# Optimization experiments

Hardware: AMD Instinct MI355X
Metric: run time of the kernel (lower is better)

The kernel has to match this reference:

```python
import jax, jax.numpy as jnp
import numpy as np

E, B, D, H, Z = 8, 16384, 512, 512, 64   # experts, batch, input_dim, hidden, latent
NHID = 2                                 # num_mlp_layers - 1 hidden-to-hidden layers


def setup_inputs() -> dict:
    key = jax.random.key(0)
    ks = jax.random.split(key, 12)

    def w(k, shape, fan_in):
        return (jax.random.normal(k, shape, jnp.float32) / np.sqrt(fan_in)).astype(jnp.float32)

    return {
        "x": jax.random.normal(ks[0], (B, D), jnp.float32),
        "eps": jax.random.normal(ks[1], (B, Z), jnp.float32),
        # stacked per-expert parameters (leading axis E)
        "enc_in_w": w(ks[2], (E, D, H), D), "enc_in_b": jnp.zeros((E, H), jnp.float32),
        "enc_hid_w": w(ks[3], (E, NHID, H, H), H), "enc_hid_b": jnp.zeros((E, NHID, H), jnp.float32),
        "mu_w": w(ks[4], (E, H, Z), H), "mu_b": jnp.zeros((E, Z), jnp.float32),
        "lv_w": w(ks[5], (E, H, Z), H), "lv_b": jnp.zeros((E, Z), jnp.float32),
        "dec_in_w": w(ks[6], (E, Z, H), Z), "dec_in_b": jnp.zeros((E, H), jnp.float32),
        "dec_hid_w": w(ks[7], (E, NHID, H, H), H), "dec_hid_b": jnp.zeros((E, NHID, H), jnp.float32),
        "dec_out_w": w(ks[8], (E, H, D), H), "dec_out_b": jnp.zeros((E, D), jnp.float32),
    }


def _moe_forward(x, eps, enc_in_w, enc_in_b, enc_hid_w, enc_hid_b,
                 mu_w, mu_b, lv_w, lv_b,
                 dec_in_w, dec_in_b, dec_hid_w, dec_hid_b, dec_out_w, dec_out_b):
    # ---- every expert tries the problem (dense, all experts over full batch) ----
    h = jax.nn.relu(jnp.einsum('bd,edh->ebh', x, enc_in_w) + enc_in_b[:, None, :])
    for i in range(NHID):
        h = jax.nn.relu(jnp.einsum('ebh,ehk->ebk', h, enc_hid_w[:, i]) + enc_hid_b[:, i, None, :])
    mu = jnp.einsum('ebh,ehz->ebz', h, mu_w) + mu_b[:, None, :]          # [E,B,Z]
    logvar = jnp.einsum('ebh,ehz->ebz', h, lv_w) + lv_b[:, None, :]       # [E,B,Z]
    z = mu + jnp.exp(0.5 * logvar) * eps[None, :, :]                      # reparameterize
    g = jax.nn.relu(jnp.einsum('ebz,ezh->ebh', z, dec_in_w) + dec_in_b[:, None, :])
    for i in range(NHID):
        g = jax.nn.relu(jnp.einsum('ebh,ehk->ebk', g, dec_hid_w[:, i]) + dec_hid_b[:, i, None, :])
    xhat = jnp.einsum('ebh,ehd->ebd', g, dec_out_w) + dec_out_b[:, None, :]  # [E,B,D]

    # ---- per-sample recon loss, pick best expert (torch.min over experts) ----
    recon = jnp.mean((xhat - x[None, :, :]) ** 2, axis=-1)                # [E,B]
    expert_idx = jnp.argmin(recon, axis=0)                                # [B]

    # ---- sparse_others: single fused gather instead of python loop ----
    bi = jnp.arange(x.shape[0])
    return mu[expert_idx, bi], logvar[expert_idx, bi], xhat[expert_idx, bi]


def reference(x, eps, enc_in_w, enc_in_b, enc_hid_w, enc_hid_b,
              mu_w, mu_b, lv_w, lv_b,
              dec_in_w, dec_in_b, dec_hid_w, dec_hid_b, dec_out_w, dec_out_b):
    return _moe_forward(x, eps, enc_in_w, enc_in_b, enc_hid_w, enc_hid_b,
                        mu_w, mu_b, lv_w, lv_b,
                        dec_in_w, dec_in_b, dec_hid_w, dec_hid_b, dec_out_w, dec_out_b)
```

## Files before the change

### kernel.cpp

```cpp
#include <hip/hip_runtime.h>
#include <cstdint>

#define Eexp 8
#define Bb   16384
#define Dd   512
#define Hh   512
#define Zz   64

typedef _Float16 f16x8 __attribute__((ext_vector_type(8)));
typedef float    f32x4 __attribute__((ext_vector_type(4)));

#define OFF_ENCIN  0
#define OFF_HID0   524288
#define OFF_HID1   1048576
#define OFF_HEADS  1572864
#define OFF_DECIN  1703936
#define OFF_DHID0  1769472
#define OFF_DHID1  2293760
#define OFF_DECOUT 2818048
#define PEREXP     3342336
#define WT_TOTAL   (8 * (size_t)PEREXP)

#define GLL16(g, l) __builtin_amdgcn_global_load_lds( \
    (const __attribute__((address_space(1))) void*)(g), \
    (__attribute__((address_space(3))) void*)(l), 16, 0, 0)

template<bool TR>
__global__ __launch_bounds__(256)
void fmsplit(const float* __restrict__ src, _Float16* __restrict__ dst,
             int KTOT, int inner, long sStride, long dStride)
{
    __shared__ float t[64][65];
    const int e  = blockIdx.z;
    const int o0 = blockIdx.x * 64;
    const int k0 = blockIdx.y * 64;
    const float* S = src + (size_t)e * sStride;
    _Float16*    D = dst + (size_t)e * dStride;
    const int tid = threadIdx.x;
    const int rr = tid >> 4, c4 = (tid & 15) * 4;
    #pragma unroll
    for (int p = 0; p < 4; ++p) {
        const int r = rr + p * 16;
        const float4 v = *reinterpret_cast<const float4*>(
            S + (size_t)(TR ? (k0 + r) : (o0 + r)) * inner + (TR ? o0 : k0) + c4);
        t[r][c4 + 0] = v.x; t[r][c4 + 1] = v.y;
        t[r][c4 + 2] = v.z; t[r][c4 + 3] = v.w;
    }
    __syncthreads();
    const int lane = tid & 63, wid = tid >> 6;
    const int KB = KTOT >> 5;
    #pragma unroll
    for (int p = 0; p < 2; ++p) {
        const int g  = wid * 2 + p;
        const int ot = g >> 1, kb = g & 1;
        const int rI = ot * 16 + (lane & 15);
        const int kI = kb * 32 + (lane >> 4) * 8;
        f16x8 hv, lv;
        #pragma unroll
        for (int j = 0; j < 8; ++j) {
            const float v = TR ? t[kI + j][rI] : t[rI][kI + j];
            const _Float16 h = (_Float16)v;
            hv[j] = h; lv[j] = (_Float16)(v - (float)h);
        }
        const size_t base = ((size_t)((o0 >> 4) + ot) * KB + (k0 >> 5) + kb) * 1024;
        *reinterpret_cast<f16x8*>(D + base + lane * 8)       = hv;
        *reinterpret_cast<f16x8*>(D + base + 512 + lane * 8) = lv;
    }
}

__global__ __launch_bounds__(256)
void zfm_kernel(const float* __restrict__ mu, const float* __restrict__ lv,
                const float* __restrict__ eps, _Float16* __restrict__ zfm)
{
    __shared__ float t[64][65];
    const int r0 = blockIdx.x * 64;
    const int tid = threadIdx.x, rr = tid >> 4, c4 = (tid & 15) * 4;
    #pragma unroll
    for (int p = 0; p < 4; ++p) {
        const int r = rr + p * 16;
        const size_t o = (size_t)(r0 + r) * 64 + c4;
        const float4 m = *reinterpret_cast<const float4*>(mu + o);
        const float4 l = *reinterpret_cast<const float4*>(lv + o);
        const float4 e = *reinterpret_cast<const float4*>(eps + o);
        t[r][c4 + 0] = m.x + expf(0.5f * l.x) * e.x;
        t[r][c4 + 1] = m.y + expf(0.5f * l.y) * e.y;
        t[r][c4 + 2] = m.z + expf(0.5f * l.z) * e.z;
        t[r][c4 + 3] = m.w + expf(0.5f * l.w) * e.w;
    }
    __syncthreads();
    const int lane = tid & 63, wid = tid >> 6;
    #pragma unroll
    for (int p = 0; p < 2; ++p) {
        const int g  = wid * 2 + p;
        const int ot = g >> 1, kb = g & 1;
        const int rI = ot * 16 + (lane & 15);
        const int kI = kb * 32 + (lane >> 4) * 8;
        f16x8 hv, lvv;
        #pragma unroll
        for (int j = 0; j < 8; ++j) {
            const float v = t[rI][kI + j];
            const _Float16 h = (_Float16)v;
            hv[j] = h; lvv[j] = (_Float16)(v - (float)h);
        }
        const size_t base = ((size_t)((r0 >> 4) + ot) * 2 + kb) * 1024;
        *reinterpret_cast<f16x8*>(zfm + base + lane * 8)       = hv;
        *reinterpret_cast<f16x8*>(zfm + base + 512 + lane * 8) = lvv;
    }
}

template<int KA, int MODE>
__global__ __launch_bounds__(256, 2)
void gemm11(const _Float16* __restrict__ Afm, const _Float16* __restrict__ Wfm,
            const float* __restrict__ bias0, const float* __restrict__ bias1,
            float* __restrict__ Cf, float* __restrict__ Cf1,
            _Float16* __restrict__ Cfm, const float* __restrict__ Xin,
            float* __restrict__ rec8)
{
    constexpr bool BIG = (MODE != 2);
    constexpr int MF  = BIG ? 4 : 2;
    constexpr int KB  = KA / 32;
    constexpr int NT  = KB;
    constexpr int ACH = BIG ? 16 : 8;
    constexpr int NCH = ACH + 16;
    constexpr int GPW = NCH / 4;
    __shared__ __align__(16) _Float16 lds[2 * NCH * 512];

    const int bid = blockIdx.x;
    int bx, by;
    if (BIG) { bx = (bid & 7) * 16 + (bid >> 5); by = (bid >> 3) & 3; }
    else     { bx = (bid & 7) * 32 + (bid >> 3); by = 0; }

    const int lane = threadIdx.x & 63, wid = threadIdx.x >> 6;
    const int wr = wid >> 1, wc = wid & 1;
    const int row0 = bx * (BIG ? 128 : 64);
    const int col0 = by * 128;

    const _Float16* src[GPW];
    #pragma unroll
    for (int p = 0; p < GPW; ++p) {
        const int q = wid * GPW + p;
        if (q < ACH)
            src[p] = Afm + (size_t)((row0 >> 4) + (q >> 1)) * KB * 1024
                         + (q & 1) * 512 + lane * 8;
        else {
            const int qq = q - ACH;
            src[p] = Wfm + (size_t)((col0 >> 4) + (qq >> 1)) * KB * 1024
                         + (qq & 1) * 512 + lane * 8;
        }
    }

    f32x4 acc[MF][4];
    #pragma unroll
    for (int i = 0; i < MF; ++i)
        #pragma unroll
        for (int j = 0; j < 4; ++j) acc[i][j] = {0.f, 0.f, 0.f, 0.f};

#define STAGE(buf)                                                           \
    { _Pragma("unroll")                                                      \
      for (int p = 0; p < GPW; ++p) {                                        \
          GLL16(src[p], lds + (buf) * (NCH * 512) + (wid * GPW + p) * 512);  \
          src[p] += 1024;                                                    \
      } }

    STAGE(0)
    if (NT > 1) STAGE(1)

    for (int t = 0; t < NT; ++t) {
        if (t + 1 < NT) { asm volatile("s_waitcnt vmcnt(%0)" :: "i"(GPW) : "memory"); }
        else            { asm volatile("s_waitcnt vmcnt(0)" ::: "memory"); }
        __builtin_amdgcn_s_barrier();
        asm volatile("" ::: "memory");

        const _Float16* B0 = lds + (t & 1) * (NCH * 512);
        f16x8 ah[MF], al[MF], wh[4], wl[4];
        #pragma unroll
        for (int mf = 0; mf < MF; ++mf) {
            const int q = (wr * MF + mf) * 2;
            ah[mf] = *reinterpret_cast<const f16x8*>(B0 + q * 512 + lane * 8);
            al[mf] = *reinterpret_cast<const f16x8*>(B0 + q * 512 + 512 + lane * 8);
        }
        #pragma unroll
        for (int nf = 0; nf < 4; ++nf) {
            const int q = ACH + (wc * 4 + nf) * 2;
            wh[nf] = *reinterpret_cast<const f16x8*>(B0 + q * 512 + lane * 8);
            wl[nf] = *reinterpret_cast<const f16x8*>(B0 + q * 512 + 512 + lane * 8);
        }
        __builtin_amdgcn_s_setprio(1);
        #pragma unroll
        for (int mf = 0; mf < MF; ++mf)
            #pragma unroll
            for (int nf = 0; nf < 4; ++nf) {
                acc[mf][nf] = __builtin_amdgcn_mfma_f32_16x16x32_f16(
                    ah[mf], wh[nf], acc[mf][nf], 0, 0, 0);
                acc[mf][nf] = __builtin_amdgcn_mfma_f32_16x16x32_f16(
                    ah[mf], wl[nf], acc[mf][nf], 0, 0, 0);
                acc[mf][nf] = __builtin_amdgcn_mfma_f32_16x16x32_f16(
                    al[mf], wh[nf], acc[mf][nf], 0, 0, 0);
            }
        __builtin_amdgcn_s_setprio(0);
        asm volatile("" ::: "memory");
        __builtin_amdgcn_s_barrier();
        asm volatile("" ::: "memory");
        if (t + 2 < NT) STAGE(t & 1)
    }
#undef STAGE

    if constexpr (MODE == 0) {
        uint32_t* sb = reinterpret_cast<uint32_t*>(&lds[0]);
        #pragma unroll
        for (int ph = 0; ph < 2; ++ph) {
            if (wc == ph) {
                #pragma unroll
                for (int nf = 0; nf < 4; ++nf) {
                    const int c_l = nf * 16 + (lane & 15);
                    const float bv = bias0[col0 + ph * 64 + c_l];
                    #pragma unroll
                    for (int mf = 0; mf < 4; ++mf)
                        #pragma unroll
                        for (int j = 0; j < 4; ++j) {
                            const int r_l = wr * 64 + mf * 16 + (lane >> 4) * 4 + j;
                            const float v = fmaxf(acc[mf][nf][j] + bv, 0.f);
                            const _Float16 h = (_Float16)v;
                            const _Float16 lo = (_Float16)(v - (float)h);
                            const uint32_t pk =
                                (uint32_t)__builtin_bit_cast(uint16_t, h) |
                                ((uint32_t)__builtin_bit_cast(uint16_t, lo) << 16);
                            sb[r_l * 64 + (((c_l >> 2) ^ (r_l & 15)) << 2) + (c_l & 3)] = pk;
                        }
                }
            }
            __syncthreads();
            {
                #pragma unroll
                for (int i = 0; i < 4; ++i) {
                    const int q = wid * 4 + i;
                    const int T_l = q >> 1, kb_l = q & 1;
                    const int r_l = T_l * 16 + (lane & 15);
                    const int cb  = kb_l * 32 + (lane >> 4) * 8;
                    uint32_t u[8];
                    #pragma unroll
                    for (int jb = 0; jb < 2; ++jb) {
                        const int chunk = ((cb >> 2) + jb) ^ (r_l & 15);
                        const uint32_t* pp = &sb[r_l * 64 + chunk * 4];
                        u[jb*4+0] = pp[0]; u[jb*4+1] = pp[1];
                        u[jb*4+2] = pp[2]; u[jb*4+3] = pp[3];
                    }
                    f16x8 hv, lvv;
                    #pragma unroll
                    for (int j = 0; j < 8; ++j) {
                        hv[j]  = __builtin_bit_cast(_Float16, (uint16_t)(u[j] & 0xffff));
                        lvv[j] = __builtin_bit_cast(_Float16, (uint16_t)(u[j] >> 16));
                    }
                    const size_t base =
                        ((size_t)((row0 >> 4) + T_l) * 16 +
                         ((col0 + ph * 64) >> 5) + kb_l) * 1024;
                    *reinterpret_cast<f16x8*>(Cfm + base + lane * 8)       = hv;
                    *reinterpret_cast<f16x8*>(Cfm + base + 512 + lane * 8) = lvv;
                }
            }
            __syncthreads();
        }
    } else if constexpr (MODE == 1) {
        float rsum[4][4];
        #pragma unroll
        for (int mf = 0; mf < 4; ++mf)
            #pragma unroll
            for (int j = 0; j < 4; ++j) rsum[mf][j] = 0.f;
        #pragma unroll
        for (int nf = 0; nf < 4; ++nf) {
            const int col = col0 + wc * 64 + nf * 16 + (lane & 15);
            const float bv = bias0[col];
            #pragma unroll
            for (int mf = 0; mf < 4; ++mf)
                #pragma unroll
                for (int j = 0; j < 4; ++j) {
                    const int row = row0 + wr * 64 + mf * 16 + (lane >> 4) * 4 + j;
                    const float v = acc[mf][nf][j] + bv;
                    Cf[(size_t)row * 512 + col] = v;
                    const float d = v - Xin[(size_t)row * 512 + col];
                    rsum[mf][j] += d * d;
                }
        }
        #pragma unroll
        for (int mf = 0; mf < 4; ++mf)
            #pragma unroll
            for (int j = 0; j < 4; ++j) {
                float s = rsum[mf][j];
                s += __shfl_xor(s, 1); s += __shfl_xor(s, 2);
                s += __shfl_xor(s, 4); s += __shfl_xor(s, 8);
                if ((lane & 15) == 0) {
                    const int row = row0 + wr * 64 + mf * 16 + (lane >> 4) * 4 + j;
                    rec8[(size_t)(by * 2 + wc) * Bb + row] = s;
                }
            }
    } else {
        #pragma unroll
        for (int nf = 0; nf < 4; ++nf) {
            const int c_h = wc * 64 + nf * 16 + (lane & 15);
            const float bv = (c_h < 64) ? bias0[c_h] : bias1[c_h - 64];
            float* CP = (c_h < 64) ? Cf : Cf1;
            const int c = c_h & 63;
            #pragma unroll
            for (int mf = 0; mf < MF; ++mf)
                #pragma unroll
                for (int j = 0; j < 4; ++j) {
                    const int row = row0 + wr * 32 + mf * 16 + (lane >> 4) * 4 + j;
                    CP[(size_t)row * 64 + c] = acc[mf][nf][j] + bv;
                }
        }
    }
}

__global__ __launch_bounds__(256)
void select_kernel(const float* __restrict__ rec8, float* __restrict__ best,
                   const float* __restrict__ mu_e, const float* __restrict__ lv_e,
                   const float* __restrict__ xhat,
                   float* __restrict__ out_mu, float* __restrict__ out_lv,
                   float* __restrict__ out_xh, int isFirst)
{
    const int wave = threadIdx.x >> 6;
    const int lane = threadIdx.x & 63;
    const int row  = blockIdx.x * 4 + wave;
    float r = 0.f;
    #pragma unroll
    for (int p = 0; p < 8; ++p) r += rec8[(size_t)p * Bb + row];
    r *= (1.0f / 512.0f);
    const bool cond = isFirst || (r < best[row]);
    if (cond) {
        if (lane == 0) best[row] = r;
        out_mu[(size_t)row * Zz + lane] = mu_e[(size_t)row * Zz + lane];
        out_lv[(size_t)row * Zz + lane] = lv_e[(size_t)row * Zz + lane];
        const float4* src = reinterpret_cast<const float4*>(&xhat[(size_t)row * Dd]);
        float4*       dst = reinterpret_cast<float4*>(&out_xh[(size_t)row * Dd]);
        dst[lane]      = src[lane];
        dst[lane + 64] = src[lane + 64];
    }
}

extern "C" void kernel_launch(void* const* d_in, const int* in_sizes, int n_in,
                              void* d_out, int out_size, void* d_ws, size_t ws_size,
                              hipStream_t stream)
{
    const float* x         = (const float*)d_in[0];
    const float* eps       = (const float*)d_in[1];
    const float* enc_in_w  = (const float*)d_in[2];
    const float* enc_in_b  = (const float*)d_in[3];
    const float* enc_hid_w = (const float*)d_in[4];
    const float* enc_hid_b = (const float*)d_in[5];
    const float* mu_w      = (const float*)d_in[6];
    const float* mu_b      = (const float*)d_in[7];
    const float* lv_w      = (const float*)d_in[8];
    const float* lv_b      = (const float*)d_in[9];
    const float* dec_in_w  = (const float*)d_in[10];
    const float* dec_in_b  = (const float*)d_in[11];
    const float* dec_hid_w = (const float*)d_in[12];
    const float* dec_hid_b = (const float*)d_in[13];
    const float* dec_out_w = (const float*)d_in[14];
    const float* dec_out_b = (const float*)d_in[15];

    const size_t FM = (size_t)Bb * 512 * 2;
    const size_t BZ = (size_t)Bb * 64;

    _Float16* wt  = (_Float16*)d_ws;
    _Float16* xfm = wt + WT_TOTAL;
    _Float16* afm = xfm + FM;
    _Float16* bfm = afm + FM;
    _Float16* zfm = bfm + FM;
    float* fbase  = (float*)(zfm + (size_t)Bb * 64 * 2);
    float* xhat   = fbase;
    float* mu_e   = xhat + (size_t)Bb * 512;
    float* lv_e   = mu_e + BZ;
    float* rec8   = lv_e + BZ;
    float* best   = rec8 + (size_t)8 * Bb;

    float* out_mu = (float*)d_out;
    float* out_lv = out_mu + (size_t)Bb * Zz;
    float* out_xh = out_lv + (size_t)Bb * Zz;

    const dim3 blk(256);

    fmsplit<true ><<<dim3(8, 8, 8), blk, 0, stream>>>(enc_in_w,           wt + OFF_ENCIN,  512, 512, 262144, PEREXP);
    fmsplit<true ><<<dim3(8, 8, 8), blk, 0, stream>>>(enc_hid_w,          wt + OFF_HID0,   512, 512, 524288, PEREXP);
    fmsplit<true ><<<dim3(8, 8, 8), blk, 0, stream>>>(enc_hid_w + 262144, wt + OFF_HID1,   512, 512, 524288, PEREXP);
    fmsplit<true ><<<dim3(1, 8, 8), blk, 0, stream>>>(mu_w,               wt + OFF_HEADS,  512,  64,  32768, PEREXP);
    fmsplit<true ><<<dim3(1, 8, 8), blk, 0, stream>>>(lv_w,        wt + OFF_HEADS + 65536, 512,  64,  32768, PEREXP);
    fmsplit<true ><<<dim3(8, 1, 8), blk, 0, stream>>>(dec_in_w,           wt + OFF_DECIN,   64, 512,  32768, PEREXP);
    fmsplit<true ><<<dim3(8, 8, 8), blk, 0, stream>>>(dec_hid_w,          wt + OFF_DHID0,  512, 512, 524288, PEREXP);
    fmsplit<true ><<<dim3(8, 8, 8), blk, 0, stream>>>(dec_hid_w + 262144, wt + OFF_DHID1,  512, 512, 524288, PEREXP);
    fmsplit<true ><<<dim3(8, 8, 8), blk, 0, stream>>>(dec_out_w,          wt + OFF_DECOUT, 512, 512, 262144, PEREXP);
    fmsplit<false><<<dim3(256, 8, 1), blk, 0, stream>>>(x,                xfm,             512, 512, 0, 0);

    const dim3 g512(512), g256(256), gRow(Bb / 4), gZ(Bb / 64);

    for (int e = 0; e < Eexp; ++e) {
        const _Float16* we = wt + (size_t)e * PEREXP;
        gemm11<512, 0><<<g512, blk, 0, stream>>>(
            xfm, we + OFF_ENCIN, enc_in_b + (size_t)e * Hh, nullptr,
            nullptr, nullptr, afm, nullptr, nullptr);
        gemm11<512, 0><<<g512, blk, 0, stream>>>(
            afm, we + OFF_HID0, enc_hid_b + ((size_t)e * 2 + 0) * Hh, nullptr,
            nullptr, nullptr, bfm, nullptr, nullptr);
        gemm11<512, 0><<<g512, blk, 0, stream>>>(
            bfm, we + OFF_HID1, enc_hid_b + ((size_t)e * 2 + 1) * Hh, nullptr,
            nullptr, nullptr, afm, nullptr, nullptr);
        gemm11<512, 2><<<g256, blk, 0, stream>>>(
            afm, we + OFF_HEADS, mu_b + (size_t)e * Zz, lv_b + (size_t)e * Zz,
            mu_e, lv_e, nullptr, nullptr, nullptr);
        zfm_kernel<<<gZ, blk, 0, stream>>>(mu_e, lv_e, eps, zfm);
        gemm11< 64, 0><<<g512, blk, 0, stream>>>(
            zfm, we + OFF_DECIN, dec_in_b + (size_t)e * Hh, nullptr,
            nullptr, nullptr, bfm, nullptr, nullptr);
        gemm11<512, 0><<<g512, blk, 0, stream>>>(
            bfm, we + OFF_DHID0, dec_hid_b + ((size_t)e * 2 + 0) * Hh, nullptr,
            nullptr, nullptr, afm, nullptr, nullptr);
        gemm11<512, 0><<<g512, blk, 0, stream>>>(
            afm, we + OFF_DHID1, dec_hid_b + ((size_t)e * 2 + 1) * Hh, nullptr,
            nullptr, nullptr, bfm, nullptr, nullptr);
        gemm11<512, 1><<<g512, blk, 0, stream>>>(
            bfm, we + OFF_DECOUT, dec_out_b + (size_t)e * Dd, nullptr,
            xhat, nullptr, nullptr, x, rec8);
        select_kernel<<<gRow, blk, 0, stream>>>(
            rec8, best, mu_e, lv_e, xhat, out_mu, out_lv, out_xh, e == 0 ? 1 : 0);
    }
}
```

Baseline: 1.737 ms.

## Fuse reparameterization into heads GEMM and argmin-select into decoder output GEMM

Folds the z = mu + exp(0.5*logvar)*eps step and its fp16 hi/lo split into the heads GEMM epilogue, which removes the separate zfm kernel and a re-read of mu/logvar. The decoder output GEMM now uses 512-thread blocks that each cover a full 64x512 row slab. This lets it compute per-row reconstruction error in-block, compare against the running best, and write the winning xhat, mu and logvar directly. The fp32 xhat and rec8 intermediates and the select kernel are dropped, cutting global traffic and launches per expert. The cost is a new tile shape and a serial per-row copy loop for mu/lv in two waves.

```diff
diff --git a/kernel.cpp b/kernel.cpp
--- a/kernel.cpp
+++ b/kernel.cpp
@@ -68,71 +68,25 @@
     }
 }
 
-__global__ __launch_bounds__(256)
-void zfm_kernel(const float* __restrict__ mu, const float* __restrict__ lv,
-                const float* __restrict__ eps, _Float16* __restrict__ zfm)
+template<int KA>
+__global__ __launch_bounds__(256, 2)
+void gemm_mid(const _Float16* __restrict__ Afm, const _Float16* __restrict__ Wfm,
+              const float* __restrict__ bias0, _Float16* __restrict__ Cfm)
 {
-    __shared__ float t[64][65];
-    const int r0 = blockIdx.x * 64;
-    const int tid = threadIdx.x, rr = tid >> 4, c4 = (tid & 15) * 4;
-    #pragma unroll
-    for (int p = 0; p < 4; ++p) {
-        const int r = rr + p * 16;
-        const size_t o = (size_t)(r0 + r) * 64 + c4;
-        const float4 m = *reinterpret_cast<const float4*>(mu + o);
-        const float4 l = *reinterpret_cast<const float4*>(lv + o);
-        const float4 e = *reinterpret_cast<const float4*>(eps + o);
-        t[r][c4 + 0] = m.x + expf(0.5f * l.x) * e.x;
-        t[r][c4 + 1] = m.y + expf(0.5f * l.y) * e.y;
-        t[r][c4 + 2] = m.z + expf(0.5f * l.z) * e.z;
-        t[r][c4 + 3] = m.w + expf(0.5f * l.w) * e.w;
-    }
-    __syncthreads();
-    const int lane = tid & 63, wid = tid >> 6;
-    #pragma unroll
-    for (int p = 0; p < 2; ++p) {
-        const int g  = wid * 2 + p;
-        const int ot = g >> 1, kb = g & 1;
-        const int rI = ot * 16 + (lane & 15);
-        const int kI = kb * 32 + (lane >> 4) * 8;
-        f16x8 hv, lvv;
-        #pragma unroll
-        for (int j = 0; j < 8; ++j) {
-            const float v = t[rI][kI + j];
-            const _Float16 h = (_Float16)v;
-            hv[j] = h; lvv[j] = (_Float16)(v - (float)h);
-        }
-        const size_t base = ((size_t)((r0 >> 4) + ot) * 2 + kb) * 1024;
-        *reinterpret_cast<f16x8*>(zfm + base + lane * 8)       = hv;
-        *reinterpret_cast<f16x8*>(zfm + base + 512 + lane * 8) = lvv;
-    }
-}
-
-template<int KA, int MODE>
-__global__ __launch_bounds__(256, 2)
-void gemm11(const _Float16* __restrict__ Afm, const _Float16* __restrict__ Wfm,
-            const float* __restrict__ bias0, const float* __restrict__ bias1,
-            float* __restrict__ Cf, float* __restrict__ Cf1,
-            _Float16* __restrict__ Cfm, const float* __restrict__ Xin,
-            float* __restrict__ rec8)
-{
-    constexpr bool BIG = (MODE != 2);
-    constexpr int MF  = BIG ? 4 : 2;
     constexpr int KB  = KA / 32;
     constexpr int NT  = KB;
-    constexpr int ACH = BIG ? 16 : 8;
-    constexpr int NCH = ACH + 16;
-    constexpr int GPW = NCH / 4;
+    constexpr int ACH = 16;
+    constexpr int NCH = 32;
+    constexpr int GPW = 8;
     __shared__ __align__(16) _Float16 lds[2 * NCH * 512];
 
     const int bid = blockIdx.x;
-    int bx, by;
-    if (BIG) { bx = (bid & 7) * 16 + (bid >> 5); by = (bid >> 3) & 3; }
-    else     { bx = (bid & 7) * 32 + (bid >> 3); by = 0; }
+    const int bx = (bid & 7) * 16 + (bid >> 5);
+    const int by = (bid >> 3) & 3;
 
     const int lane = threadIdx.x & 63, wid = threadIdx.x >> 6;
     const int wr = wid >> 1, wc = wid & 1;
-    const int row0 = bx * (BIG ? 128 : 64);
+    const int row0 = bx * 128;
     const int col0 = by * 128;
 
     const _Float16* src[GPW];
@@ -149,9 +103,9 @@
         }
     }
 
-    f32x4 acc[MF][4];
-    #pragma unroll
-    for (int i = 0; i < MF; ++i)
+    f32x4 acc[4][4];
+    #pragma unroll
+    for (int i = 0; i < 4; ++i)
         #pragma unroll
         for (int j = 0; j < 4; ++j) acc[i][j] = {0.f, 0.f, 0.f, 0.f};
 
@@ -172,10 +126,10 @@
         asm volatile("" ::: "memory");
 
         const _Float16* B0 = lds + (t & 1) * (NCH * 512);
-        f16x8 ah[MF], al[MF], wh[4], wl[4];
-        #pragma unroll
-        for (int mf = 0; mf < MF; ++mf) {
-            const int q = (wr * MF + mf) * 2;
+        f16x8 ah[4], al[4], wh[4], wl[4];
+        #pragma unroll
+        for (int mf = 0; mf < 4; ++mf) {
+            const int q = (wr * 4 + mf) * 2;
             ah[mf] = *reinterpret_cast<const f16x8*>(B0 + q * 512 + lane * 8);
             al[mf] = *reinterpret_cast<const f16x8*>(B0 + q * 512 + 512 + lane * 8);
         }
@@ -187,7 +141,7 @@
         }
         __builtin_amdgcn_s_setprio(1);
         #pragma unroll
-        for (int mf = 0; mf < MF; ++mf)
+        for (int mf = 0; mf < 4; ++mf)
             #pragma unroll
             for (int nf = 0; nf < 4; ++nf) {
                 acc[mf][nf] = __builtin_amdgcn_mfma_f32_16x16x32_f16(
@@ -205,135 +159,338 @@
     }
 #undef STAGE
 
-    if constexpr (MODE == 0) {
-        uint32_t* sb = reinterpret_cast<uint32_t*>(&lds[0]);
-        #pragma unroll
-        for (int ph = 0; ph < 2; ++ph) {
-            if (wc == ph) {
+    uint32_t* sb = reinterpret_cast<uint32_t*>(&lds[0]);
+    #pragma unroll
+    for (int ph = 0; ph < 2; ++ph) {
+        if (wc == ph) {
+            #pragma unroll
+            for (int nf = 0; nf < 4; ++nf) {
+                const int c_l = nf * 16 + (lane & 15);
+                const float bv = bias0[col0 + ph * 64 + c_l];
                 #pragma unroll
-                for (int nf = 0; nf < 4; ++nf) {
-                    const int c_l = nf * 16 + (lane & 15);
-                    const float bv = bias0[col0 + ph * 64 + c_l];
+                for (int mf = 0; mf < 4; ++mf)
                     #pragma unroll
-                    for (int mf = 0; mf < 4; ++mf)
-                        #pragma unroll
-                        for (int j = 0; j < 4; ++j) {
-                            const int r_l = wr * 64 + mf * 16 + (lane >> 4) * 4 + j;
-                            const float v = fmaxf(acc[mf][nf][j] + bv, 0.f);
-                            const _Float16 h = (_Float16)v;
-                            const _Float16 lo = (_Float16)(v - (float)h);
-                            const uint32_t pk =
-                                (uint32_t)__builtin_bit_cast(uint16_t, h) |
-                                ((uint32_t)__builtin_bit_cast(uint16_t, lo) << 16);
-                            sb[r_l * 64 + (((c_l >> 2) ^ (r_l & 15)) << 2) + (c_l & 3)] = pk;
-                        }
+                    for (int j = 0; j < 4; ++j) {
+                        const int r_l = wr * 64 + mf * 16 + (lane >> 4) * 4 + j;
+                        const float v = fmaxf(acc[mf][nf][j] + bv, 0.f);
+                        const _Float16 h = (_Float16)v;
+                        const _Float16 lo = (_Float16)(v - (float)h);
+                        const uint32_t pk =
+                            (uint32_t)__builtin_bit_cast(uint16_t, h) |
+                            ((uint32_t)__builtin_bit_cast(uint16_t, lo) << 16);
+                        sb[r_l * 64 + (((c_l >> 2) ^ (r_l & 15)) << 2) + (c_l & 3)] = pk;
+                    }
+            }
+        }
+        __syncthreads();
+        {
+            #pragma unroll
+            for (int i = 0; i < 4; ++i) {
+                const int q = wid * 4 + i;
+                const int T_l = q >> 1, kb_l = q & 1;
+                const int r_l = T_l * 16 + (lane & 15);
+                const int cb  = kb_l * 32 + (lane >> 4) * 8;
+                uint32_t u[8];
+                #pragma unroll
+                for (int jb = 0; jb < 2; ++jb) {
+                    const int chunk = ((cb >> 2) + jb) ^ (r_l & 15);
+                    const uint32_t* pp = &sb[r_l * 64 + chunk * 4];
+                    u[jb*4+0] = pp[0]; u[jb*4+1] = pp[1];
+                    u[jb*4+2] = pp[2]; u[jb*4+3] = pp[3];
                 }
-            }
-            __syncthreads();
-            {
+                f16x8 hv, lvv;
                 #pragma unroll
-                for (int i = 0; i < 4; ++i) {
-                    const int q = wid * 4 + i;
-                    const int T_l = q >> 1, kb_l = q & 1;
-                    const int r_l = T_l * 16 + (lane & 15);
-                    const int cb  = kb_l * 32 + (lane >> 4) * 8;
-                    uint32_t u[8];
-                    #pragma unroll
-                    for (int jb = 0; jb < 2; ++jb) {
-                        const int chunk = ((cb >> 2) + jb) ^ (r_l & 15);
-                        const uint32_t* pp = &sb[r_l * 64 + chunk * 4];
-                        u[jb*4+0] = pp[0]; u[jb*4+1] = pp[1];
-                        u[jb*4+2] = pp[2]; u[jb*4+3] = pp[3];
-                    }
-                    f16x8 hv, lvv;
-                    #pragma unroll
-                    for (int j = 0; j < 8; ++j) {
-                        hv[j]  = __builtin_bit_cast(_Float16, (uint16_t)(u[j] & 0xffff));
-                        lvv[j] = __builtin_bit_cast(_Float16, (uint16_t)(u[j] >> 16));
-                    }
-                    const size_t base =
-                        ((size_t)((row0 >> 4) + T_l) * 16 +
-                         ((col0 + ph * 64) >> 5) + kb_l) * 1024;
-                    *reinterpret_cast<f16x8*>(Cfm + base + lane * 8)       = hv;
-                    *reinterpret_cast<f16x8*>(Cfm + base + 512 + lane * 8) = lvv;
+                for (int j = 0; j < 8; ++j) {
+                    hv[j]  = __builtin_bit_cast(_Float16, (uint16_t)(u[j] & 0xffff));
+                    lvv[j] = __builtin_bit_cast(_Float16, (uint16_t)(u[j] >> 16));
                 }
-            }
-            __syncthreads();
-        }
-    } else if constexpr (MODE == 1) {
-        float rsum[4][4];
-        #pragma unroll
-        for (int mf = 0; mf < 4; ++mf)
-            #pragma unroll
-            for (int j = 0; j < 4; ++j) rsum[mf][j] = 0.f;
+                const size_t base =
+                    ((size_t)((row0 >> 4) + T_l) * 16 +
+                     ((col0 + ph * 64) >> 5) + kb_l) * 1024;
+                *reinterpret_cast<f16x8*>(Cfm + base + lane * 8)       = hv;
+                *reinterpret_cast<f16x8*>(Cfm + base + 512 + lane * 8) = lvv;
+            }
+        }
+        __syncthreads();
+    }
+}
+
+__global__ __launch_bounds__(256, 2)
+void heads_z(const _Float16* __restrict__ Afm, const _Float16* __restrict__ Wfm,
+             const float* __restrict__ mu_b, const float* __restrict__ lv_b,
+             const float* __restrict__ eps,
+             float* __restrict__ mu_e, float* __restrict__ lv_e,
+             _Float16* __restrict__ zfm)
+{
+    constexpr int KB = 16, NT = 16, ACH = 8, NCH = 24, GPW = 6;
+    __shared__ __align__(16) _Float16 lds[2 * NCH * 512];
+
+    const int bid = blockIdx.x;
+    const int bx = (bid & 7) * 32 + (bid >> 3);
+    const int lane = threadIdx.x & 63, wid = threadIdx.x >> 6;
+    const int wr = wid >> 1, wc = wid & 1;
+    const int row0 = bx * 64;
+
+    const _Float16* src[GPW];
+    #pragma unroll
+    for (int p = 0; p < GPW; ++p) {
+        const int q = wid * GPW + p;
+        if (q < ACH)
+            src[p] = Afm + (size_t)((row0 >> 4) + (q >> 1)) * KB * 1024
+                         + (q & 1) * 512 + lane * 8;
+        else {
+            const int qq = q - ACH;
+            src[p] = Wfm + (size_t)(qq >> 1) * KB * 1024 + (qq & 1) * 512 + lane * 8;
+        }
+    }
+
+    f32x4 acc[2][4];
+    #pragma unroll
+    for (int i = 0; i < 2; ++i)
+        #pragma unroll
+        for (int j = 0; j < 4; ++j) acc[i][j] = {0.f, 0.f, 0.f, 0.f};
+
+#define STAGE(buf)                                                           \
+    { _Pragma("unroll")                                                      \
+      for (int p = 0; p < GPW; ++p) {                                        \
+          GLL16(src[p], lds + (buf) * (NCH * 512) + (wid * GPW + p) * 512);  \
+          src[p] += 1024;                                                    \
+      } }
+
+    STAGE(0)
+    STAGE(1)
+
+    for (int t = 0; t < NT; ++t) {
+        if (t + 1 < NT) { asm volatile("s_waitcnt vmcnt(%0)" :: "i"(GPW) : "memory"); }
+        else            { asm volatile("s_waitcnt vmcnt(0)" ::: "memory"); }
+        __builtin_amdgcn_s_barrier();
+        asm volatile("" ::: "memory");
+
+        const _Float16* B0 = lds + (t & 1) * (NCH * 512);
+        f16x8 ah[2], al[2], wh[4], wl[4];
+        #pragma unroll
+        for (int mf = 0; mf < 2; ++mf) {
+            const int q = (wr * 2 + mf) * 2;
+            ah[mf] = *reinterpret_cast<const f16x8*>(B0 + q * 512 + lane * 8);
+            al[mf] = *reinterpret_cast<const f16x8*>(B0 + q * 512 + 512 + lane * 8);
+        }
         #pragma unroll
         for (int nf = 0; nf < 4; ++nf) {
-            const int col = col0 + wc * 64 + nf * 16 + (lane & 15);
-            const float bv = bias0[col];
-            #pragma unroll
-            for (int mf = 0; mf < 4; ++mf)
-                #pragma unroll
-                for (int j = 0; j < 4; ++j) {
-                    const int row = row0 + wr * 64 + mf * 16 + (lane >> 4) * 4 + j;
-                    const float v = acc[mf][nf][j] + bv;
-                    Cf[(size_t)row * 512 + col] = v;
-                    const float d = v - Xin[(size_t)row * 512 + col];
-                    rsum[mf][j] += d * d;
-                }
-        }
-        #pragma unroll
-        for (int mf = 0; mf < 4; ++mf)
+            const int q = ACH + (wc * 4 + nf) * 2;
+            wh[nf] = *reinterpret_cast<const f16x8*>(B0 + q * 512 + lane * 8);
+            wl[nf] = *reinterpret_cast<const f16x8*>(B0 + q * 512 + 512 + lane * 8);
+        }
+        __builtin_amdgcn_s_setprio(1);
+        #pragma unroll
+        for (int mf = 0; mf < 2; ++mf)
+            #pragma unroll
+            for (int nf = 0; nf < 4; ++nf) {
+                acc[mf][nf] = __builtin_amdgcn_mfma_f32_16x16x32_f16(
+                    ah[mf], wh[nf], acc[mf][nf], 0, 0, 0);
+                acc[mf][nf] = __builtin_amdgcn_mfma_f32_16x16x32_f16(
+                    ah[mf], wl[nf], acc[mf][nf], 0, 0, 0);
+                acc[mf][nf] = __builtin_amdgcn_mfma_f32_16x16x32_f16(
+                    al[mf], wh[nf], acc[mf][nf], 0, 0, 0);
+            }
+        __builtin_amdgcn_s_setprio(0);
+        asm volatile("" ::: "memory");
+        __builtin_amdgcn_s_barrier();
+        asm volatile("" ::: "memory");
+        if (t + 2 < NT) STAGE(t & 1)
+    }
+#undef STAGE
+
+    float* mulv = reinterpret_cast<float*>(&lds[0]);
+    #pragma unroll
+    for (int nf = 0; nf < 4; ++nf) {
+        const int c_h = wc * 64 + nf * 16 + (lane & 15);
+        const float bv = (c_h < 64) ? mu_b[c_h] : lv_b[c_h - 64];
+        #pragma unroll
+        for (int mf = 0; mf < 2; ++mf)
             #pragma unroll
             for (int j = 0; j < 4; ++j) {
-                float s = rsum[mf][j];
-                s += __shfl_xor(s, 1); s += __shfl_xor(s, 2);
-                s += __shfl_xor(s, 4); s += __shfl_xor(s, 8);
-                if ((lane & 15) == 0) {
-                    const int row = row0 + wr * 64 + mf * 16 + (lane >> 4) * 4 + j;
-                    rec8[(size_t)(by * 2 + wc) * Bb + row] = s;
-                }
-            }
-    } else {
-        #pragma unroll
-        for (int nf = 0; nf < 4; ++nf) {
-            const int c_h = wc * 64 + nf * 16 + (lane & 15);
-            const float bv = (c_h < 64) ? bias0[c_h] : bias1[c_h - 64];
-            float* CP = (c_h < 64) ? Cf : Cf1;
-            const int c = c_h & 63;
-            #pragma unroll
-            for (int mf = 0; mf < MF; ++mf)
-                #pragma unroll
-                for (int j = 0; j < 4; ++j) {
-                    const int row = row0 + wr * 32 + mf * 16 + (lane >> 4) * 4 + j;
-                    CP[(size_t)row * 64 + c] = acc[mf][nf][j] + bv;
-                }
-        }
+                const int r_l = wr * 32 + mf * 16 + (lane >> 4) * 4 + j;
+                mulv[r_l * 128 + c_h] = acc[mf][nf][j] + bv;
+            }
+    }
+    __syncthreads();
+    const int tid = threadIdx.x;
+    #pragma unroll
+    for (int k = 0; k < 16; ++k) {
+        const int id  = tid + k * 256;
+        const int r_l = id >> 6, c = id & 63;
+        const float m = mulv[r_l * 128 + c];
+        const float l = mulv[r_l * 128 + 64 + c];
+        const size_t go = (size_t)(row0 + r_l) * 64 + c;
+        const float ev = eps[go];
+        const float z  = m + expf(0.5f * l) * ev;
+        mu_e[go] = m; lv_e[go] = l;
+        const _Float16 h  = (_Float16)z;
+        const _Float16 lo = (_Float16)(z - (float)h);
+        const size_t base = ((size_t)((row0 + r_l) >> 4) * 2 + (c >> 5)) * 1024
+                            + ((r_l & 15) + ((c >> 3) & 3) * 16) * 8 + (c & 7);
+        zfm[base]       = h;
+        zfm[base + 512] = lo;
     }
 }
 
-__global__ __launch_bounds__(256)
-void select_kernel(const float* __restrict__ rec8, float* __restrict__ best,
+__global__ __launch_bounds__(512, 2)
+void dec_out_fused(const _Float16* __restrict__ Afm, const _Float16* __restrict__ Wfm,
+                   const float* __restrict__ bias,
+                   const float* __restrict__ Xin,
                    const float* __restrict__ mu_e, const float* __restrict__ lv_e,
-                   const float* __restrict__ xhat,
+                   float* __restrict__ best,
                    float* __restrict__ out_mu, float* __restrict__ out_lv,
                    float* __restrict__ out_xh, int isFirst)
 {
-    const int wave = threadIdx.x >> 6;
-    const int lane = threadIdx.x & 63;
-    const int row  = blockIdx.x * 4 + wave;
-    float r = 0.f;
-    #pragma unroll
-    for (int p = 0; p < 8; ++p) r += rec8[(size_t)p * Bb + row];
-    r *= (1.0f / 512.0f);
-    const bool cond = isFirst || (r < best[row]);
-    if (cond) {
-        if (lane == 0) best[row] = r;
-        out_mu[(size_t)row * Zz + lane] = mu_e[(size_t)row * Zz + lane];
-        out_lv[(size_t)row * Zz + lane] = lv_e[(size_t)row * Zz + lane];
-        const float4* src = reinterpret_cast<const float4*>(&xhat[(size_t)row * Dd]);
-        float4*       dst = reinterpret_cast<float4*>(&out_xh[(size_t)row * Dd]);
-        dst[lane]      = src[lane];
-        dst[lane + 64] = src[lane + 64];
+    constexpr int KB = 16, NT = 16, ACH = 8, NCH = 72, GPW = 9;
+    __shared__ __align__(16) _Float16 lds[2 * NCH * 512];
+
+    const int bid = blockIdx.x;
+    const int bx = (bid & 7) * 32 + (bid >> 3);
+    const int lane = threadIdx.x & 63, wid = threadIdx.x >> 6;
+    const int row0 = bx * 64;
+    const int colW = wid * 64;
+
+    const _Float16* src[GPW];
+    #pragma unroll
+    for (int p = 0; p < GPW; ++p) {
+        const int q = wid * GPW + p;
+        if (q < ACH)
+            src[p] = Afm + (size_t)((row0 >> 4) + (q >> 1)) * KB * 1024
+                         + (q & 1) * 512 + lane * 8;
+        else {
+            const int qq = q - ACH;
+            src[p] = Wfm + (size_t)(qq >> 1) * KB * 1024 + (qq & 1) * 512 + lane * 8;
+        }
+    }
+
+    f32x4 acc[4][4];
+    #pragma unroll
+    for (int i = 0; i < 4; ++i)
+        #pragma unroll
+        for (int j = 0; j < 4; ++j) acc[i][j] = {0.f, 0.f, 0.f, 0.f};
+
+#define STAGE(buf)                                                           \
+    { _Pragma("unroll")                                                      \
+      for (int p = 0; p < GPW; ++p) {                                        \
+          GLL16(src[p], lds + (buf) * (NCH * 512) + (wid * GPW + p) * 512);  \
+          src[p] += 1024;                                                    \
+      } }
+
+    STAGE(0)
+    STAGE(1)
+
+    for (int t = 0; t < NT; ++t) {
+        if (t + 1 < NT) { asm volatile("s_waitcnt vmcnt(%0)" :: "i"(GPW) : "memory"); }
+        else            { asm volatile("s_waitcnt vmcnt(0)" ::: "memory"); }
+        __builtin_amdgcn_s_barrier();
+        asm volatile("" ::: "memory");
+
+        const _Float16* B0 = lds + (t & 1) * (NCH * 512);
+        f16x8 ah[4], al[4], wh[4], wl[4];
+        #pragma unroll
+        for (int mf = 0; mf < 4; ++mf) {
+            const int q = mf * 2;
+            ah[mf] = *reinterpret_cast<const f16x8*>(B0 + q * 512 + lane * 8);
+            al[mf] = *reinterpret_cast<const f16x8*>(B0 + q * 512 + 512 + lane * 8);
+        }
+        #pragma unroll
+        for (int nf = 0; nf < 4; ++nf) {
+            const int q = ACH + (wid * 4 + nf) * 2;
+            wh[nf] = *reinterpret_cast<const f16x8*>(B0 + q * 512 + lane * 8);
+            wl[nf] = *reinterpret_cast<const f16x8*>(B0 + q * 512 + 512 + lane * 8);
+        }
+        __builtin_amdgcn_s_setprio(1);
+        #pragma unroll
+        for (int mf = 0; mf < 4; ++mf)
+            #pragma unroll
+            for (int nf = 0; nf < 4; ++nf) {
+                acc[mf][nf] = __builtin_amdgcn_mfma_f32_16x16x32_f16(
+                    ah[mf], wh[nf], acc[mf][nf], 0, 0, 0);
+                acc[mf][nf] = __builtin_amdgcn_mfma_f32_16x16x32_f16(
+                    ah[mf], wl[nf], acc[mf][nf], 0, 0, 0);
+                acc[mf][nf] = __builtin_amdgcn_mfma_f32_16x16x32_f16(
+                    al[mf], wh[nf], acc[mf][nf], 0, 0, 0);
+            }
+        __builtin_amdgcn_s_setprio(0);
+        asm volatile("" ::: "memory");
+        __builtin_amdgcn_s_barrier();
+        asm volatile("" ::: "memory");
+        if (t + 2 < NT) STAGE(t & 1)
+    }
+#undef STAGE
+
+    float*    recP = reinterpret_cast<float*>(&lds[0]);
+    int*      winf = reinterpret_cast<int*>(recP + 8 * 64);
+
+    float rsum[4][4];
+    #pragma unroll
+    for (int mf = 0; mf < 4; ++mf)
+        #pragma unroll
+        for (int j = 0; j < 4; ++j) rsum[mf][j] = 0.f;
+    float bv[4];
+    #pragma unroll
+    for (int nf = 0; nf < 4; ++nf) bv[nf] = bias[colW + nf * 16 + (lane & 15)];
+    #pragma unroll
+    for (int nf = 0; nf < 4; ++nf) {
+        const int col = colW + nf * 16 + (lane & 15);
+        #pragma unroll
+        for (int mf = 0; mf < 4; ++mf)
+            #pragma unroll
+            for (int j = 0; j < 4; ++j) {
+                const int r_l = mf * 16 + (lane >> 4) * 4 + j;
+                const float v = acc[mf][nf][j] + bv[nf];
+                const float d = v - Xin[(size_t)(row0 + r_l) * 512 + col];
+                rsum[mf][j] += d * d;
+            }
+    }
+    #pragma unroll
+    for (int mf = 0; mf < 4; ++mf)
+        #pragma unroll
+        for (int j = 0; j < 4; ++j) {
+            float s = rsum[mf][j];
+            s += __shfl_xor(s, 1); s += __shfl_xor(s, 2);
+            s += __shfl_xor(s, 4); s += __shfl_xor(s, 8);
+            if ((lane & 15) == 0)
+                recP[wid * 64 + mf * 16 + (lane >> 4) * 4 + j] = s;
+        }
+    __syncthreads();
+    if (wid == 0) {
+        float r = 0.f;
+        #pragma unroll
+        for (int w = 0; w < 8; ++w) r += recP[w * 64 + lane];
+        const int grow = row0 + lane;
+        const bool w = isFirst || (r < best[grow]);
+        if (w) best[grow] = r;
+        winf[lane] = w ? 1 : 0;
+    }
+    __syncthreads();
+    #pragma unroll
+    for (int mf = 0; mf < 4; ++mf)
+        #pragma unroll
+        for (int j = 0; j < 4; ++j) {
+            const int r_l = mf * 16 + (lane >> 4) * 4 + j;
+            if (winf[r_l]) {
+                #pragma unroll
+                for (int nf = 0; nf < 4; ++nf) {
+                    const int col = colW + nf * 16 + (lane & 15);
+                    out_xh[(size_t)(row0 + r_l) * 512 + col] = acc[mf][nf][j] + bv[nf];
+                }
+            }
+        }
+    if (wid == 0) {
+        for (int r = 0; r < 64; ++r)
+            if (winf[r]) {
+                const size_t o = (size_t)(row0 + r) * 64 + lane;
+                out_mu[o] = mu_e[o];
+            }
+    } else if (wid == 1) {
+        for (int r = 0; r < 64; ++r)
+            if (winf[r]) {
+                const size_t o = (size_t)(row0 + r) * 64 + lane;
+                out_lv[o] = lv_e[o];
+            }
     }
 }
 
@@ -367,11 +524,9 @@
     _Float16* bfm = afm + FM;
     _Float16* zfm = bfm + FM;
     float* fbase  = (float*)(zfm + (size_t)Bb * 64 * 2);
-    float* xhat   = fbase;
-    float* mu_e   = xhat + (size_t)Bb * 512;
+    float* mu_e   = fbase;
     float* lv_e   = mu_e + BZ;
-    float* rec8   = lv_e + BZ;
-    float* best   = rec8 + (size_t)8 * Bb;
+    float* best   = lv_e + BZ;
 
     float* out_mu = (float*)d_out;
     float* out_lv = out_mu + (size_t)Bb * Zz;
@@ -390,36 +545,27 @@
     fmsplit<true ><<<dim3(8, 8, 8), blk, 0, stream>>>(dec_out_w,          wt + OFF_DECOUT, 512, 512, 262144, PEREXP);
     fmsplit<false><<<dim3(256, 8, 1), blk, 0, stream>>>(x,                xfm,             512, 512, 0, 0);
 
-    const dim3 g512(512), g256(256), gRow(Bb / 4), gZ(Bb / 64);
+    const dim3 g512(512), g256(256), blk512(512);
 
     for (int e = 0; e < Eexp; ++e) {
         const _Float16* we = wt + (size_t)e * PEREXP;
-        gemm11<512, 0><<<g512, blk, 0, stream>>>(
-            xfm, we + OFF_ENCIN, enc_in_b + (size_t)e * Hh, nullptr,
-            nullptr, nullptr, afm, nullptr, nullptr);
-        gemm11<512, 0><<<g512, blk, 0, stream>>>(
-            afm, we + OFF_HID0, enc_hid_b + ((size_t)e * 2 + 0) * Hh, nullptr,
-            nullptr, nullptr, bfm, nullptr, nullptr);
-        gemm11<512, 0><<<g512, blk, 0, stream>>>(
-            bfm, we + OFF_HID1, enc_hid_b + ((size_t)e * 2 + 1) * Hh, nullptr,
-            nullptr, nullptr, afm, nullptr, nullptr);
-        gemm11<512, 2><<<g256, blk, 0, stream>>>(
+        gemm_mid<512><<<g512, blk, 0, stream>>>(
+            xfm, we + OFF_ENCIN, enc_in_b + (size_t)e * Hh, afm);
+        gemm_mid<512><<<g512, blk, 0, stream>>>(
+            afm, we + OFF_HID0, enc_hid_b + ((size_t)e * 2 + 0) * Hh, bfm);
+        gemm_mid<512><<<g512, blk, 0, stream>>>(
+            bfm, we + OFF_HID1, enc_hid_b + ((size_t)e * 2 + 1) * Hh, afm);
+        heads_z<<<g256, blk, 0, stream>>>(
             afm, we + OFF_HEADS, mu_b + (size_t)e * Zz, lv_b + (size_t)e * Zz,
-            mu_e, lv_e, nullptr, nullptr, nullptr);
-        zfm_kernel<<<gZ, blk, 0, stream>>>(mu_e, lv_e, eps, zfm);
-        gemm11< 64, 0><<<g512, blk, 0, stream>>>(
-            zfm, we + OFF_DECIN, dec_in_b + (size_t)e * Hh, nullptr,
-            nullptr, nullptr, bfm, nullptr, nullptr);
-        gemm11<512, 0><<<g512, blk, 0, stream>>>(
-            bfm, we + OFF_DHID0, dec_hid_b + ((size_t)e * 2 + 0) * Hh, nullptr,
-            nullptr, nullptr, afm, nullptr, nullptr);
-        gemm11<512, 0><<<g512, blk, 0, stream>>>(
-            afm, we + OFF_DHID1, dec_hid_b + ((size_t)e * 2 + 1) * Hh, nullptr,
-            nullptr, nullptr, bfm, nullptr, nullptr);
-        gemm11<512, 1><<<g512, blk, 0, stream>>>(
-            bfm, we + OFF_DECOUT, dec_out_b + (size_t)e * Dd, nullptr,
-            xhat, nullptr, nullptr, x, rec8);
-        select_kernel<<<gRow, blk, 0, stream>>>(
-            rec8, best, mu_e, lv_e, xhat, out_mu, out_lv, out_xh, e == 0 ? 1 : 0);
+            eps, mu_e, lv_e, zfm);
+        gemm_mid< 64><<<g512, blk, 0, stream>>>(
+            zfm, we + OFF_DECIN, dec_in_b + (size_t)e * Hh, bfm);
+        gemm_mid<512><<<g512, blk, 0, stream>>>(
+            bfm, we + OFF_DHID0, dec_hid_b + ((size_t)e * 2 + 0) * Hh, afm);
+        gemm_mid<512><<<g512, blk, 0, stream>>>(
+            afm, we + OFF_DHID1, dec_hid_b + ((size_t)e * 2 + 1) * Hh, bfm);
+        dec_out_fused<<<g256, blk512, 0, stream>>>(
+            bfm, we + OFF_DECOUT, dec_out_b + (size_t)e * Dd,
+            x, mu_e, lv_e, best, out_mu, out_lv, out_xh, e == 0 ? 1 : 0);
     }
 }
```

Measured after the change: 1.757 ms. Within noise of the previous version (+1.2%).
